# Performance work log

Measured on AMD Instinct MI355X. Metric: run time of the kernel, lower is better.

The kernel has to match this reference:

```python
import jax, jax.numpy as jnp
import numpy as np

B = 4096
ED = 128          # EMBEDDING_DIM
HD = 64           # HIDDEN_DIM
LH = 128          # LSTM_HIDDEN_DIM
IN_DIM = ED * (12 + 48 + 1)  # 7808
N_ABILITY, N_MOVE = 300, 900


def setup_inputs() -> dict:
    key = jax.random.key(0)
    ks = jax.random.split(key, 16)
    s = lambda k, shape, scale=0.05: (jax.random.normal(k, shape, dtype=jnp.float32) * scale)
    return {
        "ability_ids": jax.random.randint(ks[0], (B, 12), 0, N_ABILITY),
        "move_ids": jax.random.randint(ks[1], (B, 48), 0, N_MOVE),
        "numerical": s(ks[2], (B, 84), 1.0),
        "mask": (jax.random.uniform(ks[3], (B, 9)) > 0.3).astype(jnp.float32),
        "h0": jnp.zeros((B, LH), jnp.float32),
        "c0": jnp.zeros((B, LH), jnp.float32),
        "ability_emb": s(ks[4], (N_ABILITY, ED), 1.0),
        "move_emb": s(ks[5], (N_MOVE, ED), 1.0),
        "num_W": s(ks[6], (ED, 84)),
        "num_b": s(ks[7], (ED,)),
        "Wih": s(ks[8], (4 * LH, IN_DIM), 0.01),
        "Whh": s(ks[9], (4 * LH, LH)),
        "bih": s(ks[10], (4 * LH,)),
        "bhh": s(ks[11], (4 * LH,)),
        "W1": s(ks[12], (HD, LH)),
        "b1": s(ks[13], (HD,)),
        "W2": s(ks[14], (ED, HD)),
        "b2": s(ks[15], (ED,)),
        "Wa": s(jax.random.fold_in(key, 100), (9, ED)),
        "ba": s(jax.random.fold_in(key, 101), (9,)),
    }


def reference(ability_ids, move_ids, numerical, mask, h0, c0,
              ability_emb, move_emb, num_W, num_b,
              Wih, Whh, bih, bhh, W1, b1, W2, b2, Wa, ba):
    # Gather + concat: [B, 12*ED] + [B, 48*ED] + [B, ED] -> [B, 7808]
    ab = ability_emb[ability_ids].reshape(ability_ids.shape[0], 12 * ED)
    mv = move_emb[move_ids].reshape(move_ids.shape[0], 48 * ED)
    num = numerical @ num_W.T + num_b
    x = jnp.concatenate([ab, mv, num], axis=-1)

    # Single-timestep LSTM (torch gate order: i, f, g, o)
    gates = x @ Wih.T + bih + h0 @ Whh.T + bhh
    i, f, g, o = jnp.split(gates, 4, axis=-1)
    i, f, o = jax.nn.sigmoid(i), jax.nn.sigmoid(f), jax.nn.sigmoid(o)
    g = jnp.tanh(g)
    c1 = f * c0 + i * g
    h1 = o * jnp.tanh(c1)

    # MLP head + action logits
    feat = jax.nn.relu(h1 @ W1.T + b1) @ W2.T + b2
    probs = jax.nn.softmax(feat @ Wa.T + ba, axis=-1)

    # Masked renormalization; fall back to unmasked probs when mask kills everything
    masked = probs * mask
    ssum = masked.sum(-1, keepdims=True)
    out = jnp.where(ssum > 0, masked / jnp.where(ssum > 0, ssum, 1.0), probs)
    return out, h1, c1
```

## Files before the change

### kernel.cpp

```cpp
#include <hip/hip_runtime.h>
#include <hip/hip_bf16.h>
#include <stdint.h>
#include <stddef.h>

typedef __bf16 bf16;
typedef __bf16 bf16x8 __attribute__((ext_vector_type(8)));
typedef float f32x4 __attribute__((ext_vector_type(4)));

#define BATCH 4096
#define KIH 7808
#define KTOT 7936
#define NG 512
#define LH 128
#define HD 64
#define ED 128
#define SPLITK 4

#define OFF_WCAT 0u
#define OFF_GPART 8126464u
#define OFF_XT   24903680u
#define OFF_AB   27000832u
#define OFF_MV   27077632u
#define OFF_ADDR 27308032u
#define OFF_H1B  28356608u
#define OFF_W1F  29405184u
#define OFF_W2F  29421568u
#define OFF_WAF  29437952u
#define OFF_NB   29442048u

#define O_H1 (BATCH * 9)
#define O_C1 (BATCH * 9 + BATCH * LH)

typedef const __attribute__((address_space(1))) uint32_t* gas_ptr;
typedef __attribute__((address_space(3))) uint32_t* las_ptr;

__device__ __forceinline__ void async16(const void* g, void* l) {
    __builtin_amdgcn_global_load_lds((gas_ptr)g, (las_ptr)l, 16, 0, 0);
}

__global__ void prep(const int* __restrict__ ab_ids,
                     const int* __restrict__ mv_ids,
                     const float* __restrict__ numerical,
                     const float* __restrict__ h0,
                     const float* __restrict__ numW,
                     const float* __restrict__ numb,
                     const float* __restrict__ Wih,
                     const float* __restrict__ Whh,
                     const float* __restrict__ ab_emb,
                     const float* __restrict__ mv_emb,
                     const float* __restrict__ W1,
                     const float* __restrict__ W2,
                     const float* __restrict__ Wa,
                     uint8_t* __restrict__ ws) {
    const int bid = blockIdx.x;
    const int t = threadIdx.x;

    if (bid < BATCH) {
        bf16* xtail = (bf16*)(ws + OFF_XT);
        uint32_t* addrs = (uint32_t*)(ws + OFF_ADDR);
        const int b = bid;

        __shared__ int ids[60];
        if (t < 60) ids[t] = (t < 12) ? ab_ids[b * 12 + t] : mv_ids[b * 48 + (t - 12)];

        if (t < 128) {
            const float v = (t < 84) ? numerical[(size_t)b * 84 + t] : 0.f;
            xtail[(size_t)b * 256 + t] = (bf16)v;
        } else {
            const int tt = t - 128;
            xtail[(size_t)b * 256 + 128 + tt] = (bf16)h0[(size_t)b * LH + tt];
        }
        __syncthreads();

        if (t < 64) {
            uint32_t off;
            if (t < 12) off = OFF_AB + (uint32_t)ids[t] * 256u;
            else if (t < 60) off = OFF_MV + (uint32_t)ids[t] * 256u;
            else if (t == 60) off = OFF_XT + (uint32_t)b * 512u;
            else if (t == 61) off = OFF_XT + (uint32_t)b * 512u + 256u;
            else off = OFF_XT;
            addrs[(size_t)b * 64 + t] = off;
        }
    } else if (bid < BATCH + 512) {
        bf16* Wcat = (bf16*)(ws + OFF_WCAT);
        float* nbias = (float*)(ws + OFF_NB);
        const int n = bid - BATCH;

        __shared__ float wrow[128];
        __shared__ float nbs[128];
        if (t < 128) wrow[t] = Wih[(size_t)n * KIH + 7680 + t];
        else nbs[t - 128] = numb[t - 128];
        __syncthreads();

        const float* src_ih = Wih + (size_t)n * KIH;
        bf16* dst = Wcat + (size_t)n * KTOT;
        for (int k4 = t; k4 < 1920; k4 += 256) {
            const int k = k4 * 4;
            const float4 v = *(const float4*)(src_ih + k);
            bf16 o0 = (bf16)v.x, o1 = (bf16)v.y, o2 = (bf16)v.z, o3 = (bf16)v.w;
            dst[k] = o0; dst[k + 1] = o1; dst[k + 2] = o2; dst[k + 3] = o3;
        }
        if (t < 84) {
            float acc = 0.f;
#pragma unroll 4
            for (int e = 0; e < 128; ++e)
                acc += wrow[e] * numW[e * 84 + t];
            dst[7680 + t] = (bf16)acc;
        } else if (t < 128) {
            dst[7680 + t] = (bf16)0.f;
        } else {
            const int tt = t - 128;
            dst[KIH + tt] = (bf16)Whh[(size_t)n * LH + tt];
        }
        if (t == 255) {
            float a = 0.f;
#pragma unroll 4
            for (int e = 0; e < 128; ++e) a += wrow[e] * nbs[e];
            nbias[n] = a;
        }
    } else if (bid < BATCH + 512 + 600) {
        bf16* ab8 = (bf16*)(ws + OFF_AB);
        bf16* mv8 = (bf16*)(ws + OFF_MV);
        const int i = (bid - BATCH - 512) * 256 + t;
        if (i < 300 * 128) ab8[i] = (bf16)ab_emb[i];
        else if (i < 1200 * 128) mv8[i - 300 * 128] = (bf16)mv_emb[i - 300 * 128];
    } else {
        bf16* W1f = (bf16*)(ws + OFF_W1F);
        bf16* W2f = (bf16*)(ws + OFF_W2F);
        bf16* Waf = (bf16*)(ws + OFF_WAF);
        for (int e = t; e < 8192; e += 256) {
            const int j = e & 7, ln = (e >> 3) & 63, fid = e >> 9;
            const int kt = fid & 3, nt = fid >> 2;
            const int n = nt * 16 + (ln & 15);
            const int k = kt * 32 + (ln >> 4) * 8 + j;
            W1f[e] = (bf16)W1[n * 128 + k];
        }
        for (int e = t; e < 8192; e += 256) {
            const int j = e & 7, ln = (e >> 3) & 63, fid = e >> 9;
            const int kt = fid & 1, nt = fid >> 1;
            const int n = nt * 16 + (ln & 15);
            const int k = kt * 32 + (ln >> 4) * 8 + j;
            W2f[e] = (bf16)W2[n * 64 + k];
        }
        for (int e = t; e < 2048; e += 256) {
            const int j = e & 7, ln = (e >> 3) & 63, kt = e >> 9;
            const int n = ln & 15;
            const int k = kt * 32 + (ln >> 4) * 8 + j;
            Waf[e] = (n < 9) ? (bf16)Wa[n * 128 + k] : (bf16)0.f;
        }
    }
}

__global__ __launch_bounds__(256, 2) void gemm_gates(
    const uint8_t* __restrict__ wsbase,
    const bf16* __restrict__ Wcat,
    const uint32_t* __restrict__ addrs,
    bf16* __restrict__ gpart) {
    __shared__ bf16 As[2][128 * 64];
    __shared__ bf16 Bs[2][128 * 64];
    __shared__ uint32_t adr[17][128];

    const int tid = threadIdx.x;
    const int w = tid >> 6;
    const int lane = tid & 63;
    const int bm = blockIdx.x;
    const int bn = blockIdx.y;
    const int bz = blockIdx.z;
    const int kt_beg = bz * 31;
    const int kt_end = kt_beg + 31;

    const int s0 = kt_beg >> 1;
    const int ns = ((kt_end - 1) >> 1) - s0 + 1;
    for (int i = tid; i < ns * 128; i += 256) {
        adr[i >> 7][i & 127] =
            addrs[(size_t)(bm * 128 + (i & 127)) * 64 + s0 + (i >> 7)];
    }

    const int r_l = lane >> 3;
    const int sc16 = ((lane & 7) ^ r_l) * 16;

    const int wn = w & 1;
    const int wk = w >> 1;
    const int n0 = wn * 64;
    const int kk8 = wk * 4 + (lane >> 4);
    const int fl = lane & 15;

    f32x4 acc[8][4];
#pragma unroll
    for (int i = 0; i < 8; ++i)
#pragma unroll
        for (int j = 0; j < 4; ++j)
#pragma unroll
            for (int r = 0; r < 4; ++r) acc[i][j][r] = 0.f;

    __syncthreads();

    auto stage = [&](int kt, int pb) {
        const int k0 = kt * 64;
        const int sl = (kt >> 1) - s0;
        const int hb = (kt & 1) * 128;
#pragma unroll
        for (int j = 0; j < 4; ++j) {
            const int row = (w * 4 + j) * 8 + r_l;
            const uint8_t* gsrc = wsbase + adr[sl][row] + hb + sc16;
            async16(gsrc, (void*)&As[pb][((w * 4 + j) * 64 + lane) * 8]);
        }
#pragma unroll
        for (int j = 0; j < 4; ++j) {
            const int row = (w * 4 + j) * 8 + r_l;
            const bf16* gsrc = Wcat + (size_t)(bn * 128 + row) * KTOT + k0 + (sc16 >> 1);
            async16(gsrc, (void*)&Bs[pb][((w * 4 + j) * 64 + lane) * 8]);
        }
    };

    stage(kt_beg, 0);

    for (int kt = kt_beg; kt < kt_end; ++kt) {
        const int pb = (kt - kt_beg) & 1;
        __syncthreads();
        if (kt + 1 < kt_end) stage(kt + 1, pb ^ 1);

        const bf16* Ab = &As[pb][0];
        const bf16* Bb = &Bs[pb][0];

        bf16x8 bfr[4];
#pragma unroll
        for (int tj = 0; tj < 4; ++tj) {
            const int n = n0 + tj * 16 + fl;
            bfr[tj] = *(const bf16x8*)&Bb[n * 64 + ((kk8 ^ (n & 7)) * 8)];
        }
#pragma unroll
        for (int ti = 0; ti < 8; ++ti) {
            const int m = ti * 16 + fl;
            const bf16x8 af = *(const bf16x8*)&Ab[m * 64 + ((kk8 ^ (m & 7)) * 8)];
#pragma unroll
            for (int tj = 0; tj < 4; ++tj)
                acc[ti][tj] = __builtin_amdgcn_mfma_f32_16x16x32_bf16(
                    af, bfr[tj], acc[ti][tj], 0, 0, 0);
        }
    }

    __syncthreads();
    float* red = (wn == 0) ? (float*)&As[0][0] : (float*)&Bs[0][0];
    if (wk == 1) {
#pragma unroll
        for (int ti = 0; ti < 8; ++ti)
#pragma unroll
            for (int tj = 0; tj < 4; ++tj)
#pragma unroll
                for (int r = 0; r < 4; ++r)
                    red[((ti * 4 + tj) * 4 + r) * 64 + lane] = acc[ti][tj][r];
    }
    __syncthreads();

    if (wk == 0) {
        bf16* gdst = gpart + (size_t)bz * BATCH * NG;
        const int mlo = (lane >> 4) * 4;
#pragma unroll
        for (int ti = 0; ti < 8; ++ti)
#pragma unroll
            for (int tj = 0; tj < 4; ++tj) {
                const int mg = bm * 128 + ti * 16 + mlo;
                const int ng = bn * 128 + n0 + tj * 16 + fl;
                bf16* dst = gdst + (size_t)mg * NG + ng;
#pragma unroll
                for (int r = 0; r < 4; ++r)
                    dst[(size_t)r * NG] = (bf16)(
                        acc[ti][tj][r] + red[((ti * 4 + tj) * 4 + r) * 64 + lane]);
            }
    }
}

__global__ void reduce_lstm(const bf16* __restrict__ gpart,
                            const float* __restrict__ bih,
                            const float* __restrict__ bhh,
                            const float* __restrict__ nbias,
                            const float* __restrict__ c0,
                            float* __restrict__ out,
                            bf16* __restrict__ h1b) {
    const int t = threadIdx.x;
    const int b = blockIdx.x * 2 + (t >> 7);
    const int u = t & 127;

    float gv[4];
#pragma unroll
    for (int q = 0; q < 4; ++q)
        gv[q] = bih[q * 128 + u] + bhh[q * 128 + u] + nbias[q * 128 + u];
#pragma unroll
    for (int z = 0; z < SPLITK; ++z) {
        const bf16* gz = gpart + ((size_t)z * BATCH + b) * NG + u;
#pragma unroll
        for (int q = 0; q < 4; ++q) gv[q] += (float)gz[q * 128];
    }

    const float iv = 1.f / (1.f + __expf(-gv[0]));
    const float fv = 1.f / (1.f + __expf(-gv[1]));
    const float gg = tanhf(gv[2]);
    const float ov = 1.f / (1.f + __expf(-gv[3]));
    const float c1 = fv * c0[(size_t)b * LH + u] + iv * gg;
    const float h1 = ov * tanhf(c1);

    out[O_H1 + (size_t)b * LH + u] = h1;
    out[O_C1 + (size_t)b * LH + u] = c1;
    h1b[(size_t)b * LH + u] = (bf16)h1;
}

__global__ __launch_bounds__(64) void mlp_head(
    const bf16* __restrict__ h1b, const float* __restrict__ mask,
    const bf16* __restrict__ W1f, const bf16* __restrict__ W2f,
    const bf16* __restrict__ Waf,
    const float* __restrict__ b1, const float* __restrict__ b2,
    const float* __restrict__ ba,
    float* __restrict__ out) {
    __shared__ bf16 uS[16 * 64];
    __shared__ bf16 fS[16 * 128];

    const int lane = threadIdx.x;
    const int b0 = blockIdx.x * 16;
    const int nl = lane & 15, kg = lane >> 4;

    bf16x8 ah[4];
#pragma unroll
    for (int kt = 0; kt < 4; ++kt)
        ah[kt] = *(const bf16x8*)&h1b[(size_t)(b0 + nl) * 128 + kt * 32 + kg * 8];

#pragma unroll
    for (int nt = 0; nt < 4; ++nt) {
        f32x4 a = {0.f, 0.f, 0.f, 0.f};
#pragma unroll
        for (int kt = 0; kt < 4; ++kt)
            a = __builtin_amdgcn_mfma_f32_16x16x32_bf16(
                ah[kt], *(const bf16x8*)&W1f[((nt * 4 + kt) * 64 + lane) * 8],
                a, 0, 0, 0);
        const int n = nt * 16 + nl;
        const float bb = b1[n];
#pragma unroll
        for (int r = 0; r < 4; ++r)
            uS[(kg * 4 + r) * 64 + n] = (bf16)fmaxf(a[r] + bb, 0.f);
    }
    __syncthreads();

    bf16x8 au[2];
#pragma unroll
    for (int kt = 0; kt < 2; ++kt)
        au[kt] = *(const bf16x8*)&uS[nl * 64 + kt * 32 + kg * 8];

#pragma unroll
    for (int nt = 0; nt < 8; ++nt) {
        f32x4 a = {0.f, 0.f, 0.f, 0.f};
#pragma unroll
        for (int kt = 0; kt < 2; ++kt)
            a = __builtin_amdgcn_mfma_f32_16x16x32_bf16(
                au[kt], *(const bf16x8*)&W2f[((nt * 2 + kt) * 64 + lane) * 8],
                a, 0, 0, 0);
        const int n = nt * 16 + nl;
        const float bb = b2[n];
#pragma unroll
        for (int r = 0; r < 4; ++r)
            fS[(kg * 4 + r) * 128 + n] = (bf16)(a[r] + bb);
    }
    __syncthreads();

    bf16x8 afr[4];
#pragma unroll
    for (int kt = 0; kt < 4; ++kt)
        afr[kt] = *(const bf16x8*)&fS[nl * 128 + kt * 32 + kg * 8];

    f32x4 lg4 = {0.f, 0.f, 0.f, 0.f};
#pragma unroll
    for (int kt = 0; kt < 4; ++kt)
        lg4 = __builtin_amdgcn_mfma_f32_16x16x32_bf16(
            afr[kt], *(const bf16x8*)&Waf[(kt * 64 + lane) * 8], lg4, 0, 0, 0);

    const float bav = (nl < 9) ? ba[nl] : 0.f;

#pragma unroll
    for (int r = 0; r < 4; ++r) {
        const int b = b0 + kg * 4 + r;
        float lg = (nl < 9) ? lg4[r] + bav : -1e30f;
        float mx = lg;
#pragma unroll
        for (int off = 1; off < 16; off <<= 1)
            mx = fmaxf(mx, __shfl_xor(mx, off, 64));
        const float e = (nl < 9) ? __expf(lg - mx) : 0.f;
        const float mv = (nl < 9) ? mask[(size_t)b * 9 + nl] : 0.f;
        float tot = e, ms = e * mv;
#pragma unroll
        for (int off = 1; off < 16; off <<= 1) {
            tot += __shfl_xor(tot, off, 64);
            ms += __shfl_xor(ms, off, 64);
        }
        if (nl < 9)
            out[(size_t)b * 9 + nl] = (ms > 0.f) ? e * mv / ms : e / tot;
    }
}

extern "C" void kernel_launch(void* const* d_in, const int* in_sizes, int n_in,
                              void* d_out, int out_size, void* d_ws, size_t ws_size,
                              hipStream_t stream) {
    const int* ab_ids = (const int*)d_in[0];
    const int* mv_ids = (const int*)d_in[1];
    const float* numerical = (const float*)d_in[2];
    const float* mask = (const float*)d_in[3];
    const float* h0 = (const float*)d_in[4];
    const float* c0 = (const float*)d_in[5];
    const float* ab_emb = (const float*)d_in[6];
    const float* mv_emb = (const float*)d_in[7];
    const float* numW = (const float*)d_in[8];
    const float* numb = (const float*)d_in[9];
    const float* Wih = (const float*)d_in[10];
    const float* Whh = (const float*)d_in[11];
    const float* bih = (const float*)d_in[12];
    const float* bhh = (const float*)d_in[13];
    const float* W1 = (const float*)d_in[14];
    const float* b1 = (const float*)d_in[15];
    const float* W2 = (const float*)d_in[16];
    const float* b2 = (const float*)d_in[17];
    const float* Wa = (const float*)d_in[18];
    const float* ba = (const float*)d_in[19];
    float* out = (float*)d_out;

    uint8_t* ws = (uint8_t*)d_ws;
    bf16* Wcat = (bf16*)(ws + OFF_WCAT);
    bf16* gpart = (bf16*)(ws + OFF_GPART);
    uint32_t* addrs = (uint32_t*)(ws + OFF_ADDR);
    bf16* h1b = (bf16*)(ws + OFF_H1B);
    bf16* W1f = (bf16*)(ws + OFF_W1F);
    bf16* W2f = (bf16*)(ws + OFF_W2F);
    bf16* Waf = (bf16*)(ws + OFF_WAF);
    float* nbias = (float*)(ws + OFF_NB);

    prep<<<BATCH + 512 + 600 + 1, 256, 0, stream>>>(
        ab_ids, mv_ids, numerical, h0, numW, numb, Wih, Whh, ab_emb, mv_emb,
        W1, W2, Wa, ws);
    gemm_gates<<<dim3(32, 4, SPLITK), 256, 0, stream>>>(ws, Wcat, addrs, gpart);
    reduce_lstm<<<BATCH / 2, 256, 0, stream>>>(gpart, bih, bhh, nbias, c0,
                                               out, h1b);
    mlp_head<<<BATCH / 16, 64, 0, stream>>>(h1b, mask, W1f, W2f, Waf,
                                            b1, b2, ba, out);
}
```

Baseline: 171.4 us.

## Fuse LSTM reduction and MLP head into one tail kernel

Merges the split-K gate reduction and LSTM cell with the MLP head and masked softmax in a single kernel that handles two batch rows per block. The h1 bf16 round trip through global memory and one kernel launch go away. In exchange, the MFMA-based head becomes scalar FP32 dot products over bf16 weights, with many idle threads in the later stages, so per-block compute and weight re-reads from cache go up.

```diff
diff --git a/kernel.cpp b/kernel.cpp
--- a/kernel.cpp
+++ b/kernel.cpp
@@ -22,11 +22,10 @@
 #define OFF_AB   27000832u
 #define OFF_MV   27077632u
 #define OFF_ADDR 27308032u
-#define OFF_H1B  28356608u
-#define OFF_W1F  29405184u
-#define OFF_W2F  29421568u
-#define OFF_WAF  29437952u
-#define OFF_NB   29442048u
+#define OFF_W1B  28356608u
+#define OFF_W2B  28372992u
+#define OFF_WAB  28389376u
+#define OFF_NB   28391680u
 
 #define O_H1 (BATCH * 9)
 #define O_C1 (BATCH * 9 + BATCH * LH)
@@ -125,29 +124,12 @@
         if (i < 300 * 128) ab8[i] = (bf16)ab_emb[i];
         else if (i < 1200 * 128) mv8[i - 300 * 128] = (bf16)mv_emb[i - 300 * 128];
     } else {
-        bf16* W1f = (bf16*)(ws + OFF_W1F);
-        bf16* W2f = (bf16*)(ws + OFF_W2F);
-        bf16* Waf = (bf16*)(ws + OFF_WAF);
-        for (int e = t; e < 8192; e += 256) {
-            const int j = e & 7, ln = (e >> 3) & 63, fid = e >> 9;
-            const int kt = fid & 3, nt = fid >> 2;
-            const int n = nt * 16 + (ln & 15);
-            const int k = kt * 32 + (ln >> 4) * 8 + j;
-            W1f[e] = (bf16)W1[n * 128 + k];
-        }
-        for (int e = t; e < 8192; e += 256) {
-            const int j = e & 7, ln = (e >> 3) & 63, fid = e >> 9;
-            const int kt = fid & 1, nt = fid >> 1;
-            const int n = nt * 16 + (ln & 15);
-            const int k = kt * 32 + (ln >> 4) * 8 + j;
-            W2f[e] = (bf16)W2[n * 64 + k];
-        }
-        for (int e = t; e < 2048; e += 256) {
-            const int j = e & 7, ln = (e >> 3) & 63, kt = e >> 9;
-            const int n = ln & 15;
-            const int k = kt * 32 + (ln >> 4) * 8 + j;
-            Waf[e] = (n < 9) ? (bf16)Wa[n * 128 + k] : (bf16)0.f;
-        }
+        bf16* W1b = (bf16*)(ws + OFF_W1B);
+        bf16* W2b = (bf16*)(ws + OFF_W2B);
+        bf16* Wab = (bf16*)(ws + OFF_WAB);
+        for (int e = t; e < 8192; e += 256) W1b[e] = (bf16)W1[e];
+        for (int e = t; e < 8192; e += 256) W2b[e] = (bf16)W2[e];
+        for (int e = t; e < 1152; e += 256) Wab[e] = (bf16)Wa[e];
     }
 }
 
@@ -271,127 +253,102 @@
     }
 }
 
-__global__ void reduce_lstm(const bf16* __restrict__ gpart,
-                            const float* __restrict__ bih,
-                            const float* __restrict__ bhh,
-                            const float* __restrict__ nbias,
-                            const float* __restrict__ c0,
-                            float* __restrict__ out,
-                            bf16* __restrict__ h1b) {
+__global__ void tail(const bf16* __restrict__ gpart,
+                     const float* __restrict__ bih,
+                     const float* __restrict__ bhh,
+                     const float* __restrict__ nbias,
+                     const float* __restrict__ c0,
+                     const float* __restrict__ mask,
+                     const bf16* __restrict__ W1b,
+                     const float* __restrict__ b1,
+                     const bf16* __restrict__ W2b,
+                     const float* __restrict__ b2,
+                     const bf16* __restrict__ Wab,
+                     const float* __restrict__ ba,
+                     float* __restrict__ out) {
+    __shared__ float h1s[2][128];
+    __shared__ float uS[2][64];
+    __shared__ float fS[2][128];
+    __shared__ float ls[2][12];
+
     const int t = threadIdx.x;
-    const int b = blockIdx.x * 2 + (t >> 7);
-    const int u = t & 127;
-
-    float gv[4];
-#pragma unroll
-    for (int q = 0; q < 4; ++q)
-        gv[q] = bih[q * 128 + u] + bhh[q * 128 + u] + nbias[q * 128 + u];
-#pragma unroll
-    for (int z = 0; z < SPLITK; ++z) {
-        const bf16* gz = gpart + ((size_t)z * BATCH + b) * NG + u;
-#pragma unroll
-        for (int q = 0; q < 4; ++q) gv[q] += (float)gz[q * 128];
-    }
-
-    const float iv = 1.f / (1.f + __expf(-gv[0]));
-    const float fv = 1.f / (1.f + __expf(-gv[1]));
-    const float gg = tanhf(gv[2]);
-    const float ov = 1.f / (1.f + __expf(-gv[3]));
-    const float c1 = fv * c0[(size_t)b * LH + u] + iv * gg;
-    const float h1 = ov * tanhf(c1);
-
-    out[O_H1 + (size_t)b * LH + u] = h1;
-    out[O_C1 + (size_t)b * LH + u] = c1;
-    h1b[(size_t)b * LH + u] = (bf16)h1;
-}
-
-__global__ __launch_bounds__(64) void mlp_head(
-    const bf16* __restrict__ h1b, const float* __restrict__ mask,
-    const bf16* __restrict__ W1f, const bf16* __restrict__ W2f,
-    const bf16* __restrict__ Waf,
-    const float* __restrict__ b1, const float* __restrict__ b2,
-    const float* __restrict__ ba,
-    float* __restrict__ out) {
-    __shared__ bf16 uS[16 * 64];
-    __shared__ bf16 fS[16 * 128];
-
-    const int lane = threadIdx.x;
-    const int b0 = blockIdx.x * 16;
-    const int nl = lane & 15, kg = lane >> 4;
-
-    bf16x8 ah[4];
-#pragma unroll
-    for (int kt = 0; kt < 4; ++kt)
-        ah[kt] = *(const bf16x8*)&h1b[(size_t)(b0 + nl) * 128 + kt * 32 + kg * 8];
-
-#pragma unroll
-    for (int nt = 0; nt < 4; ++nt) {
-        f32x4 a = {0.f, 0.f, 0.f, 0.f};
-#pragma unroll
-        for (int kt = 0; kt < 4; ++kt)
-            a = __builtin_amdgcn_mfma_f32_16x16x32_bf16(
-                ah[kt], *(const bf16x8*)&W1f[((nt * 4 + kt) * 64 + lane) * 8],
-                a, 0, 0, 0);
-        const int n = nt * 16 + nl;
-        const float bb = b1[n];
-#pragma unroll
-        for (int r = 0; r < 4; ++r)
-            uS[(kg * 4 + r) * 64 + n] = (bf16)fmaxf(a[r] + bb, 0.f);
-    }
-    __syncthreads();
-
-    bf16x8 au[2];
-#pragma unroll
-    for (int kt = 0; kt < 2; ++kt)
-        au[kt] = *(const bf16x8*)&uS[nl * 64 + kt * 32 + kg * 8];
-
-#pragma unroll
-    for (int nt = 0; nt < 8; ++nt) {
-        f32x4 a = {0.f, 0.f, 0.f, 0.f};
-#pragma unroll
-        for (int kt = 0; kt < 2; ++kt)
-            a = __builtin_amdgcn_mfma_f32_16x16x32_bf16(
-                au[kt], *(const bf16x8*)&W2f[((nt * 2 + kt) * 64 + lane) * 8],
-                a, 0, 0, 0);
-        const int n = nt * 16 + nl;
-        const float bb = b2[n];
-#pragma unroll
-        for (int r = 0; r < 4; ++r)
-            fS[(kg * 4 + r) * 128 + n] = (bf16)(a[r] + bb);
-    }
-    __syncthreads();
-
-    bf16x8 afr[4];
-#pragma unroll
-    for (int kt = 0; kt < 4; ++kt)
-        afr[kt] = *(const bf16x8*)&fS[nl * 128 + kt * 32 + kg * 8];
-
-    f32x4 lg4 = {0.f, 0.f, 0.f, 0.f};
-#pragma unroll
-    for (int kt = 0; kt < 4; ++kt)
-        lg4 = __builtin_amdgcn_mfma_f32_16x16x32_bf16(
-            afr[kt], *(const bf16x8*)&Waf[(kt * 64 + lane) * 8], lg4, 0, 0, 0);
-
-    const float bav = (nl < 9) ? ba[nl] : 0.f;
-
-#pragma unroll
-    for (int r = 0; r < 4; ++r) {
-        const int b = b0 + kg * 4 + r;
-        float lg = (nl < 9) ? lg4[r] + bav : -1e30f;
-        float mx = lg;
-#pragma unroll
-        for (int off = 1; off < 16; off <<= 1)
-            mx = fmaxf(mx, __shfl_xor(mx, off, 64));
-        const float e = (nl < 9) ? __expf(lg - mx) : 0.f;
-        const float mv = (nl < 9) ? mask[(size_t)b * 9 + nl] : 0.f;
-        float tot = e, ms = e * mv;
-#pragma unroll
-        for (int off = 1; off < 16; off <<= 1) {
-            tot += __shfl_xor(tot, off, 64);
-            ms += __shfl_xor(ms, off, 64);
-        }
-        if (nl < 9)
-            out[(size_t)b * 9 + nl] = (ms > 0.f) ? e * mv / ms : e / tot;
+    const int b0 = blockIdx.x * 2;
+
+    {
+        const int b = b0 + (t >> 7);
+        const int u = t & 127;
+        float gv[4];
+#pragma unroll
+        for (int q = 0; q < 4; ++q)
+            gv[q] = bih[q * 128 + u] + bhh[q * 128 + u] + nbias[q * 128 + u];
+#pragma unroll
+        for (int z = 0; z < SPLITK; ++z) {
+            const bf16* gz = gpart + ((size_t)z * BATCH + b) * NG + u;
+#pragma unroll
+            for (int q = 0; q < 4; ++q) gv[q] += (float)gz[q * 128];
+        }
+        const float iv = 1.f / (1.f + __expf(-gv[0]));
+        const float fv = 1.f / (1.f + __expf(-gv[1]));
+        const float gg = tanhf(gv[2]);
+        const float ov = 1.f / (1.f + __expf(-gv[3]));
+        const float c1 = fv * c0[(size_t)b * LH + u] + iv * gg;
+        const float h1 = ov * tanhf(c1);
+        out[O_H1 + (size_t)b * LH + u] = h1;
+        out[O_C1 + (size_t)b * LH + u] = c1;
+        h1s[t >> 7][u] = h1;
+    }
+    __syncthreads();
+
+    if (t < 128) {
+        const int r = t >> 6, j = t & 63;
+        float acc = b1[j];
+        const bf16* wr = W1b + j * 128;
+#pragma unroll 8
+        for (int d = 0; d < 128; ++d)
+            acc += h1s[r][d] * (float)wr[d];
+        uS[r][j] = fmaxf(acc, 0.f);
+    }
+    __syncthreads();
+
+    {
+        const int r = t >> 7, n = t & 127;
+        float acc = b2[n];
+        const bf16* wr = W2b + n * 64;
+#pragma unroll 8
+        for (int j = 0; j < 64; ++j)
+            acc += uS[r][j] * (float)wr[j];
+        fS[r][n] = acc;
+    }
+    __syncthreads();
+
+    if (t < 18) {
+        const int r = t / 9, a = t % 9;
+        float acc = ba[a];
+        const bf16* wr = Wab + a * 128;
+#pragma unroll 8
+        for (int d = 0; d < 128; ++d)
+            acc += fS[r][d] * (float)wr[d];
+        ls[r][a] = acc;
+    }
+    __syncthreads();
+
+    if (t < 2) {
+        const int b = b0 + t;
+        float mx = ls[t][0];
+#pragma unroll
+        for (int a = 1; a < 9; ++a) mx = fmaxf(mx, ls[t][a]);
+        float es[9], tot = 0.f, ms = 0.f;
+#pragma unroll
+        for (int a = 0; a < 9; ++a) {
+            es[a] = __expf(ls[t][a] - mx);
+            tot += es[a];
+            ms += es[a] * mask[(size_t)b * 9 + a];
+        }
+#pragma unroll
+        for (int a = 0; a < 9; ++a) {
+            const float mv = mask[(size_t)b * 9 + a];
+            out[(size_t)b * 9 + a] = (ms > 0.f) ? es[a] * mv / ms : es[a] / tot;
+        }
     }
 }
 
@@ -424,18 +381,15 @@
     bf16* Wcat = (bf16*)(ws + OFF_WCAT);
     bf16* gpart = (bf16*)(ws + OFF_GPART);
     uint32_t* addrs = (uint32_t*)(ws + OFF_ADDR);
-    bf16* h1b = (bf16*)(ws + OFF_H1B);
-    bf16* W1f = (bf16*)(ws + OFF_W1F);
-    bf16* W2f = (bf16*)(ws + OFF_W2F);
-    bf16* Waf = (bf16*)(ws + OFF_WAF);
+    bf16* W1b = (bf16*)(ws + OFF_W1B);
+    bf16* W2b = (bf16*)(ws + OFF_W2B);
+    bf16* Wab = (bf16*)(ws + OFF_WAB);
     float* nbias = (float*)(ws + OFF_NB);
 
     prep<<<BATCH + 512 + 600 + 1, 256, 0, stream>>>(
         ab_ids, mv_ids, numerical, h0, numW, numb, Wih, Whh, ab_emb, mv_emb,
         W1, W2, Wa, ws);
     gemm_gates<<<dim3(32, 4, SPLITK), 256, 0, stream>>>(ws, Wcat, addrs, gpart);
-    reduce_lstm<<<BATCH / 2, 256, 0, stream>>>(gpart, bih, bhh, nbias, c0,
-                                               out, h1b);
-    mlp_head<<<BATCH / 16, 64, 0, stream>>>(h1b, mask, W1f, W2f, Waf,
-                                            b1, b2, ba, out);
-}
+    tail<<<BATCH / 2, 256, 0, stream>>>(gpart, bih, bhh, nbias, c0, mask,
+                                        W1b, b1, W2b, b2, Wab, ba, out);
+}
```

Result: slower. 178.6 us (+4.2%).
